# Kernel tuning notes

Measured on AMD Instinct MI355X. Metric: run time of the kernel, lower is better.

Reference implementation:

```python
import jax, jax.numpy as jnp
import numpy as np

B, S, T, D = 16, 512, 16, 128
LN_EPS = 1e-5


def setup_inputs() -> dict:
    key = jax.random.key(0)
    k_x, k_h, k_w = jax.random.split(key, 3)
    x = jax.random.normal(k_x, (B, S, T, D), dtype=jnp.float32)
    # prev_hidden must be strictly positive (code takes its log)
    prev_hidden = jax.random.uniform(k_h, (B, 1, T, D), dtype=jnp.float32) * 0.9 + 0.05
    ln_gamma = jnp.ones((D,), jnp.float32)
    ln_beta = jnp.zeros((D,), jnp.float32)
    # torch Linear(dim, 2*dim): store as (D, 2D) for x @ W
    W = jax.random.normal(k_w, (D, 2 * D), dtype=jnp.float32) * (1.0 / np.sqrt(D))
    b = jnp.zeros((2 * D,), jnp.float32)
    return {"x": x, "prev_hidden": prev_hidden, "ln_gamma": ln_gamma,
            "ln_beta": ln_beta, "W": W, "b": b}


def _g_act_log(h):
    # log of G activation: x>=0 -> log(relu(x)+0.5); x<0 -> -softplus(-x)
    return jnp.where(h >= 0, jnp.log(jax.nn.relu(h) + 0.5), -jax.nn.softplus(-h))


def reference(x, prev_hidden, ln_gamma, ln_beta, W, b):
    seq_len = x.shape[1]
    # LayerNorm over last dim
    mu = jnp.mean(x, axis=-1, keepdims=True)
    var = jnp.var(x, axis=-1, keepdims=True)
    xn = (x - mu) * jax.lax.rsqrt(var + LN_EPS) * ln_gamma + ln_beta
    gh = jnp.einsum('bstd,de->bste', xn, W) + b  # (B,S,T,2D)
    gate, hidden = jnp.split(gh, 2, axis=-1)
    # parallel (seq_len > 1) log-space path
    log_coeffs = -jax.nn.softplus(gate)          # log(1 - z)
    log_z = -jax.nn.softplus(-gate)              # log z
    log_values = log_z + _g_act_log(hidden)      # (B,S,T,D)
    # prepend prev_hidden: values get log(h0), coeffs get zero pad
    log_values = jnp.concatenate([jnp.log(prev_hidden), log_values], axis=1)
    zero_pad = jnp.zeros_like(log_coeffs[:, :1])
    log_coeffs = jnp.concatenate([zero_pad, log_coeffs], axis=1)
    # Heinsen associative scan in log space
    a_star = jnp.cumsum(log_coeffs, axis=1)
    log_h0_plus_b_star = jax.lax.cumlogsumexp(log_values - a_star, axis=1)
    out = jnp.exp(a_star + log_h0_plus_b_star)
    out = out[:, -seq_len:]
    next_prev_hidden = out[:, -1:]
    return out, next_prev_hidden
```

## Files before the change

kernel.cpp:

```cpp
#include <hip/hip_runtime.h>
#include <hip/hip_bf16.h>
#include <stdint.h>

#define BB 16
#define SS 512
#define TT 16
#define DD 128
#define CH 32
#define NCH (SS/CH)
#define LN_EPS 1e-5f

typedef __attribute__((ext_vector_type(8))) short short8;
typedef __attribute__((ext_vector_type(4))) float f32x4;

static __device__ __forceinline__ unsigned short f2bf(float f) {
    unsigned int u = __float_as_uint(f);
    u += 0x7fffu + ((u >> 16) & 1u);
    return (unsigned short)(u >> 16);
}

static __device__ __forceinline__ uint32_t cvt_pk_bf16(float lo, float hi) {
    uint32_t r;
    asm("v_cvt_pk_bf16_f32 %0, %1, %2" : "=v"(r) : "v"(lo), "v"(hi));
    return r;
}

static __device__ __forceinline__ void dma16(const float* g, unsigned char* l) {
    __builtin_amdgcn_global_load_lds(
        (const __attribute__((address_space(1))) unsigned int*)g,
        (__attribute__((address_space(3))) unsigned int*)l, 16, 0, 0);
}

#define BAR() do {                                            \
    asm volatile("s_waitcnt lgkmcnt(0)" ::: "memory");        \
    __builtin_amdgcn_s_barrier();                             \
    asm volatile("" ::: "memory");                            \
} while (0)

__global__ __launch_bounds__(256) void k0_pack(
    const float* __restrict__ W, const float* __restrict__ gamma,
    const float* __restrict__ beta, const float* __restrict__ bias,
    unsigned short* __restrict__ wf, float* __restrict__ bp)
{
    if (blockIdx.x < 128) {
        const int id   = blockIdx.x * 256 + threadIdx.x;
        const int j    = id & 7;
        const int lane = (id >> 3) & 63;
        const int kt   = (id >> 9) & 3;
        const int nt   = (id >> 11) & 15;
        const int col  = nt*16 + (lane & 15);
        const int k    = kt*32 + (lane >> 4)*8 + j;
        wf[id] = f2bf(gamma[k] * W[(size_t)k*256 + col]);
    } else {
        const int col = threadIdx.x;
        float s = bias[col];
        #pragma unroll 8
        for (int k = 0; k < 128; ++k)
            s = fmaf(beta[k], W[(size_t)k*256 + col], s);
        bp[col] = s;
    }
}

__global__ __launch_bounds__(768, 1) void fused_mingru(
    const float* __restrict__ x, const float* __restrict__ prevh,
    const unsigned short* __restrict__ wfrag, const float* __restrict__ bp,
    float* __restrict__ out, float* __restrict__ nexth)
{
    __shared__ __align__(16) unsigned char Xb[3][CH*512];
    __shared__ __align__(16) unsigned char xnb[2][CH*256];
    __shared__ __align__(16) float2 cvb[2][CH][DD];

    const int tid  = threadIdx.x;
    const int w    = tid >> 6;
    const int lane = tid & 63;
    const int l15  = lane & 15;
    const int lhi  = lane >> 4;

    const size_t rowstride = (size_t)TT * DD;
    const size_t base_bt   = ((size_t)(blockIdx.x >> 4) * SS * TT + (blockIdx.x & 15)) * DD;

    const int gw = w - 4;
    short8 wfr[2][4];
    float  bs2[2];
    if (w >= 4) {
        #pragma unroll
        for (int ni = 0; ni < 2; ++ni) {
            const int nt = ni ? (8 + gw) : gw;
            #pragma unroll
            for (int kt = 0; kt < 4; ++kt)
                wfr[ni][kt] = *(const short8*)(wfrag + (size_t)(((nt*4+kt)*64 + lane)*8));
        }
        bs2[0] = bp[gw*16 + l15];
        bs2[1] = bp[128 + gw*16 + l15];
    }

    float h = 0.0f;
    if (tid < 128) h = prevh[(size_t)blockIdx.x * 128 + tid];

    const int tid2 = tid & 127;
    const int r_a  = tid2 >> 2;
    const int q_a  = tid2 & 3;
    const int rx   = r_a & 7;

    auto stageX = [&](int ch) {
        unsigned char* dst = Xb[ch % 3];
        const int j0 = (w == 2) ? 0 : 8;
        #pragma unroll
        for (int jj = 0; jj < 8; ++jj) {
            const int j  = j0 + jj;
            const int r  = 2*j + (lane >> 5);
            const int cc = lane & 31;
            const float* src = x + base_bt + (size_t)(ch*CH + r)*rowstride
                                 + (((cc ^ (r & 7)) << 2));
            dma16(src, dst + j*1024);
        }
    };

    auto phaseLN = [&](int st) {
        const unsigned char* xr = Xb[st % 3] + r_a*512;
        f32x4 vv[8];
        #pragma unroll
        for (int k = 0; k < 8; ++k)
            vv[k] = *(const f32x4*)(xr + (((q_a*8 + k) ^ rx) << 4));
        float s1 = 0.f, s2 = 0.f;
        #pragma unroll
        for (int k = 0; k < 8; ++k) {
            s1 += vv[k].x + vv[k].y + vv[k].z + vv[k].w;
            s2 += vv[k].x*vv[k].x + vv[k].y*vv[k].y + vv[k].z*vv[k].z + vv[k].w*vv[k].w;
        }
        s1 += __shfl_xor(s1, 1); s2 += __shfl_xor(s2, 1);
        s1 += __shfl_xor(s1, 2); s2 += __shfl_xor(s2, 2);
        const float mu = s1 * (1.0f/128.0f);
        const float rs = rsqrtf(s2 * (1.0f/128.0f) - mu*mu + LN_EPS);
        unsigned char* row = xnb[st & 1] + r_a*256;
        #pragma unroll
        for (int m = 0; m < 4; ++m) {
            const f32x4 a = vv[2*m], b = vv[2*m+1];
            union { short8 s8; uint32_t u[4]; } sv;
            sv.u[0] = cvt_pk_bf16((a.x - mu)*rs, (a.y - mu)*rs);
            sv.u[1] = cvt_pk_bf16((a.z - mu)*rs, (a.w - mu)*rs);
            sv.u[2] = cvt_pk_bf16((b.x - mu)*rs, (b.y - mu)*rs);
            sv.u[3] = cvt_pk_bf16((b.z - mu)*rs, (b.w - mu)*rs);
            *(short8*)(row + (((q_a*4 + m) ^ rx) << 4)) = sv.s8;
        }
    };

    auto phaseG = [&](int st) {
        const int bx = st & 1;
        #pragma unroll
        for (int mt = 0; mt < 2; ++mt) {
            const unsigned char* rowp = xnb[bx] + (mt*16 + l15)*256;
            short8 af[4];
            #pragma unroll
            for (int kt = 0; kt < 4; ++kt) {
                const int c = (kt << 2) | lhi;
                af[kt] = *(const short8*)(rowp + ((c ^ (l15 & 7)) << 4));
            }
            f32x4 ag = (f32x4)(0.f), ah = (f32x4)(0.f);
            #pragma unroll
            for (int kt = 0; kt < 4; ++kt) {
                ag = __builtin_amdgcn_mfma_f32_16x16x32_bf16(af[kt], wfr[0][kt], ag, 0, 0, 0);
                ah = __builtin_amdgcn_mfma_f32_16x16x32_bf16(af[kt], wfr[1][kt], ah, 0, 0, 0);
            }
            const int d = gw*16 + l15;
            #pragma unroll
            for (int j = 0; j < 4; ++j) {
                const int ls = mt*16 + lhi*4 + j;
                const float g  = ag[j] + bs2[0];
                const float hh = ah[j] + bs2[1];
                const float c  = 1.0f / (1.0f + __expf(g));
                const float ga = (hh >= 0.0f) ? (hh + 0.5f)
                                              : (1.0f / (1.0f + __expf(-hh)));
                cvb[bx][ls][d] = make_float2(c, (1.0f - c) * ga);
            }
        }
    };

    auto phaseC = [&](int st) {
        const int bc = st & 1;
        float* op = out + base_bt + (size_t)st * CH * rowstride + tid;
        #pragma unroll 8
        for (int ls = 0; ls < CH; ++ls) {
            const float2 cv = cvb[bc][ls][tid];
            h = fmaf(cv.x, h, cv.y);
            op[(size_t)ls * rowstride] = h;
        }
    };

    if (w == 2 || w == 3) { stageX(0); stageX(1); }

    for (int st = 0; st <= NCH + 1; ++st) {
        if (w >= 4) {
            if (st >= 1 && st <= NCH) phaseG(st - 1);
        } else if (w >= 2) {
            if (st < NCH) {
                if (st + 1 < NCH) asm volatile("s_waitcnt vmcnt(8)" ::: "memory");
                else              asm volatile("s_waitcnt vmcnt(0)" ::: "memory");
                phaseLN(st);
                if (st + 2 < NCH) stageX(st + 2);
            }
        } else {
            if (st >= 2) phaseC(st - 2);
        }
        BAR();
    }
    if (tid < 128) nexth[(size_t)blockIdx.x * 128 + tid] = h;
}

extern "C" void kernel_launch(void* const* d_in, const int* in_sizes, int n_in,
                              void* d_out, int out_size, void* d_ws, size_t ws_size,
                              hipStream_t stream) {
    const float* x     = (const float*)d_in[0];
    const float* prevh = (const float*)d_in[1];
    const float* gamma = (const float*)d_in[2];
    const float* beta  = (const float*)d_in[3];
    const float* W     = (const float*)d_in[4];
    const float* bias  = (const float*)d_in[5];

    float* out   = (float*)d_out;
    float* nexth = out + (size_t)BB*SS*TT*DD;

    unsigned short* wf  = (unsigned short*)d_ws;
    float*          bpf = (float*)((char*)d_ws + 65536);

    k0_pack<<<129, 256, 0, stream>>>(W, gamma, beta, bias, wf, bpf);
    fused_mingru<<<BB*TT, 768, 0, stream>>>(x, prevh, wf, bpf, out, nexth);
}
```

Before: 47.59 us.

## Fuse weight packing into main kernel and do scan in registers via MFMA lanes

```diff
diff --git a/kernel.cpp b/kernel.cpp
--- a/kernel.cpp
+++ b/kernel.cpp
@@ -6,29 +6,17 @@
 #define SS 512
 #define TT 16
 #define DD 128
-#define CH 32
+#define CH 64
 #define NCH (SS/CH)
 #define LN_EPS 1e-5f
 
 typedef __attribute__((ext_vector_type(8))) short short8;
 typedef __attribute__((ext_vector_type(4))) float f32x4;
 
-static __device__ __forceinline__ unsigned short f2bf(float f) {
-    unsigned int u = __float_as_uint(f);
-    u += 0x7fffu + ((u >> 16) & 1u);
-    return (unsigned short)(u >> 16);
-}
-
 static __device__ __forceinline__ uint32_t cvt_pk_bf16(float lo, float hi) {
     uint32_t r;
     asm("v_cvt_pk_bf16_f32 %0, %1, %2" : "=v"(r) : "v"(lo), "v"(hi));
     return r;
-}
-
-static __device__ __forceinline__ void dma16(const float* g, unsigned char* l) {
-    __builtin_amdgcn_global_load_lds(
-        (const __attribute__((address_space(1))) unsigned int*)g,
-        (__attribute__((address_space(3))) unsigned int*)l, 16, 0, 0);
 }
 
 #define BAR() do {                                            \
@@ -37,38 +25,13 @@
     asm volatile("" ::: "memory");                            \
 } while (0)
 
-__global__ __launch_bounds__(256) void k0_pack(
-    const float* __restrict__ W, const float* __restrict__ gamma,
-    const float* __restrict__ beta, const float* __restrict__ bias,
-    unsigned short* __restrict__ wf, float* __restrict__ bp)
-{
-    if (blockIdx.x < 128) {
-        const int id   = blockIdx.x * 256 + threadIdx.x;
-        const int j    = id & 7;
-        const int lane = (id >> 3) & 63;
-        const int kt   = (id >> 9) & 3;
-        const int nt   = (id >> 11) & 15;
-        const int col  = nt*16 + (lane & 15);
-        const int k    = kt*32 + (lane >> 4)*8 + j;
-        wf[id] = f2bf(gamma[k] * W[(size_t)k*256 + col]);
-    } else {
-        const int col = threadIdx.x;
-        float s = bias[col];
-        #pragma unroll 8
-        for (int k = 0; k < 128; ++k)
-            s = fmaf(beta[k], W[(size_t)k*256 + col], s);
-        bp[col] = s;
-    }
-}
-
-__global__ __launch_bounds__(768, 1) void fused_mingru(
+__global__ __launch_bounds__(512, 2) void fused_mingru(
     const float* __restrict__ x, const float* __restrict__ prevh,
-    const unsigned short* __restrict__ wfrag, const float* __restrict__ bp,
+    const float* __restrict__ gamma, const float* __restrict__ beta,
+    const float* __restrict__ W, const float* __restrict__ bias,
     float* __restrict__ out, float* __restrict__ nexth)
 {
-    __shared__ __align__(16) unsigned char Xb[3][CH*512];
     __shared__ __align__(16) unsigned char xnb[2][CH*256];
-    __shared__ __align__(16) float2 cvb[2][CH][DD];
 
     const int tid  = threadIdx.x;
     const int w    = tid >> 6;
@@ -76,80 +39,83 @@
     const int l15  = lane & 15;
     const int lhi  = lane >> 4;
 
+    const int bt = blockIdx.x;
     const size_t rowstride = (size_t)TT * DD;
-    const size_t base_bt   = ((size_t)(blockIdx.x >> 4) * SS * TT + (blockIdx.x & 15)) * DD;
+    const size_t base_bt   = ((size_t)(bt >> 4) * SS * TT + (bt & 15)) * DD;
 
-    const int gw = w - 4;
+    const int r_ln  = tid >> 3;
+    const int c8    = tid & 7;
+    const int rx_ln = r_ln & 7;
+    const float* xp0 = x + base_bt + (size_t)r_ln * rowstride + c8*16;
+
+    f32x4 px0, px1, px2, px3;
+    auto issuePx = [&](int st) {
+        const float* xp = xp0 + (size_t)st * CH * rowstride;
+        px0 = *(const f32x4*)(xp + 0);
+        px1 = *(const f32x4*)(xp + 4);
+        px2 = *(const f32x4*)(xp + 8);
+        px3 = *(const f32x4*)(xp + 12);
+    };
+    issuePx(0);
+
     short8 wfr[2][4];
     float  bs2[2];
-    if (w >= 4) {
+    #pragma unroll
+    for (int ni = 0; ni < 2; ++ni) {
+        const int col = (ni ? 128 : 0) + w*16 + l15;
+        float acc = 0.0f;
         #pragma unroll
-        for (int ni = 0; ni < 2; ++ni) {
-            const int nt = ni ? (8 + gw) : gw;
+        for (int kt = 0; kt < 4; ++kt) {
+            union { short8 s8; uint32_t u[4]; } fr;
             #pragma unroll
-            for (int kt = 0; kt < 4; ++kt)
-                wfr[ni][kt] = *(const short8*)(wfrag + (size_t)(((nt*4+kt)*64 + lane)*8));
+            for (int p = 0; p < 4; ++p) {
+                const int k0 = kt*32 + lhi*8 + 2*p;
+                const float w0 = W[(size_t)k0*256 + col];
+                const float w1 = W[(size_t)(k0+1)*256 + col];
+                acc = fmaf(beta[k0],   w0, acc);
+                acc = fmaf(beta[k0+1], w1, acc);
+                fr.u[p] = cvt_pk_bf16(gamma[k0]*w0, gamma[k0+1]*w1);
+            }
+            wfr[ni][kt] = fr.s8;
         }
-        bs2[0] = bp[gw*16 + l15];
-        bs2[1] = bp[128 + gw*16 + l15];
+        acc += __shfl_xor(acc, 16);
+        acc += __shfl_xor(acc, 32);
+        bs2[ni] = bias[col] + acc;
     }
 
-    float h = 0.0f;
-    if (tid < 128) h = prevh[(size_t)blockIdx.x * 128 + tid];
-
-    const int tid2 = tid & 127;
-    const int r_a  = tid2 >> 2;
-    const int q_a  = tid2 & 3;
-    const int rx   = r_a & 7;
-
-    auto stageX = [&](int ch) {
-        unsigned char* dst = Xb[ch % 3];
-        const int j0 = (w == 2) ? 0 : 8;
-        #pragma unroll
-        for (int jj = 0; jj < 8; ++jj) {
-            const int j  = j0 + jj;
-            const int r  = 2*j + (lane >> 5);
-            const int cc = lane & 31;
-            const float* src = x + base_bt + (size_t)(ch*CH + r)*rowstride
-                                 + (((cc ^ (r & 7)) << 2));
-            dma16(src, dst + j*1024);
-        }
-    };
+    float hM = prevh[(size_t)bt*128 + w*16 + l15];
 
     auto phaseLN = [&](int st) {
-        const unsigned char* xr = Xb[st % 3] + r_a*512;
-        f32x4 vv[8];
-        #pragma unroll
-        for (int k = 0; k < 8; ++k)
-            vv[k] = *(const f32x4*)(xr + (((q_a*8 + k) ^ rx) << 4));
-        float s1 = 0.f, s2 = 0.f;
-        #pragma unroll
-        for (int k = 0; k < 8; ++k) {
-            s1 += vv[k].x + vv[k].y + vv[k].z + vv[k].w;
-            s2 += vv[k].x*vv[k].x + vv[k].y*vv[k].y + vv[k].z*vv[k].z + vv[k].w*vv[k].w;
-        }
+        float s1 = px0.x+px0.y+px0.z+px0.w + px1.x+px1.y+px1.z+px1.w
+                 + px2.x+px2.y+px2.z+px2.w + px3.x+px3.y+px3.z+px3.w;
+        float s2 = px0.x*px0.x+px0.y*px0.y+px0.z*px0.z+px0.w*px0.w
+                 + px1.x*px1.x+px1.y*px1.y+px1.z*px1.z+px1.w*px1.w
+                 + px2.x*px2.x+px2.y*px2.y+px2.z*px2.z+px2.w*px2.w
+                 + px3.x*px3.x+px3.y*px3.y+px3.z*px3.z+px3.w*px3.w;
         s1 += __shfl_xor(s1, 1); s2 += __shfl_xor(s2, 1);
         s1 += __shfl_xor(s1, 2); s2 += __shfl_xor(s2, 2);
+        s1 += __shfl_xor(s1, 4); s2 += __shfl_xor(s2, 4);
         const float mu = s1 * (1.0f/128.0f);
         const float rs = rsqrtf(s2 * (1.0f/128.0f) - mu*mu + LN_EPS);
-        unsigned char* row = xnb[st & 1] + r_a*256;
-        #pragma unroll
-        for (int m = 0; m < 4; ++m) {
-            const f32x4 a = vv[2*m], b = vv[2*m+1];
-            union { short8 s8; uint32_t u[4]; } sv;
-            sv.u[0] = cvt_pk_bf16((a.x - mu)*rs, (a.y - mu)*rs);
-            sv.u[1] = cvt_pk_bf16((a.z - mu)*rs, (a.w - mu)*rs);
-            sv.u[2] = cvt_pk_bf16((b.x - mu)*rs, (b.y - mu)*rs);
-            sv.u[3] = cvt_pk_bf16((b.z - mu)*rs, (b.w - mu)*rs);
-            *(short8*)(row + (((q_a*4 + m) ^ rx) << 4)) = sv.s8;
-        }
+        unsigned char* row = xnb[st & 1] + r_ln*256;
+        union { short8 s8; uint32_t u[4]; } a, b2;
+        a.u[0]  = cvt_pk_bf16((px0.x-mu)*rs, (px0.y-mu)*rs);
+        a.u[1]  = cvt_pk_bf16((px0.z-mu)*rs, (px0.w-mu)*rs);
+        a.u[2]  = cvt_pk_bf16((px1.x-mu)*rs, (px1.y-mu)*rs);
+        a.u[3]  = cvt_pk_bf16((px1.z-mu)*rs, (px1.w-mu)*rs);
+        b2.u[0] = cvt_pk_bf16((px2.x-mu)*rs, (px2.y-mu)*rs);
+        b2.u[1] = cvt_pk_bf16((px2.z-mu)*rs, (px2.w-mu)*rs);
+        b2.u[2] = cvt_pk_bf16((px3.x-mu)*rs, (px3.y-mu)*rs);
+        b2.u[3] = cvt_pk_bf16((px3.z-mu)*rs, (px3.w-mu)*rs);
+        *(short8*)(row + (((2*c8)     ^ rx_ln) << 4)) = a.s8;
+        *(short8*)(row + (((2*c8 + 1) ^ rx_ln) << 4)) = b2.s8;
     };
 
     auto phaseG = [&](int st) {
-        const int bx = st & 1;
+        const unsigned char* xb = xnb[st & 1];
         #pragma unroll
-        for (int mt = 0; mt < 2; ++mt) {
-            const unsigned char* rowp = xnb[bx] + (mt*16 + l15)*256;
+        for (int mt = 0; mt < 4; ++mt) {
+            const unsigned char* rowp = xb + (mt*16 + l15)*256;
             short8 af[4];
             #pragma unroll
             for (int kt = 0; kt < 4; ++kt) {
@@ -162,49 +128,52 @@
                 ag = __builtin_amdgcn_mfma_f32_16x16x32_bf16(af[kt], wfr[0][kt], ag, 0, 0, 0);
                 ah = __builtin_amdgcn_mfma_f32_16x16x32_bf16(af[kt], wfr[1][kt], ah, 0, 0, 0);
             }
-            const int d = gw*16 + l15;
+            float Lc[4], Lv[4];
             #pragma unroll
             for (int j = 0; j < 4; ++j) {
-                const int ls = mt*16 + lhi*4 + j;
                 const float g  = ag[j] + bs2[0];
                 const float hh = ah[j] + bs2[1];
-                const float c  = 1.0f / (1.0f + __expf(g));
+                const float cc = 1.0f / (1.0f + __expf(g));
                 const float ga = (hh >= 0.0f) ? (hh + 0.5f)
                                               : (1.0f / (1.0f + __expf(-hh)));
-                cvb[bx][ls][d] = make_float2(c, (1.0f - c) * ga);
+                const float vv = (1.0f - cc) * ga;
+                if (j == 0) { Lc[0] = cc; Lv[0] = vv; }
+                else        { Lc[j] = cc * Lc[j-1]; Lv[j] = fmaf(cc, Lv[j-1], vv); }
             }
+            float Ic = Lc[3], Iv = Lv[3];
+            float pc = __shfl_up(Ic, 16), pv = __shfl_up(Iv, 16);
+            if (lhi >= 1) { Iv = fmaf(Ic, pv, Iv); Ic *= pc; }
+            pc = __shfl_up(Ic, 32); pv = __shfl_up(Iv, 32);
+            if (lhi >= 2) { Iv = fmaf(Ic, pv, Iv); Ic *= pc; }
+            float Ec = __shfl_up(Ic, 16), Ev = __shfl_up(Iv, 16);
+            if (lhi == 0) { Ec = 1.0f; Ev = 0.0f; }
+            const float Mc = __shfl(Ic, 48 + l15);
+            const float Mv = __shfl(Iv, 48 + l15);
+            const float hE = fmaf(Ec, hM, Ev);
+            float* op = out + base_bt
+                      + (size_t)(st*CH + mt*16 + lhi*4) * rowstride + w*16 + l15;
+            #pragma unroll
+            for (int j = 0; j < 4; ++j)
+                op[(size_t)j * rowstride] = fmaf(Lc[j], hE, Lv[j]);
+            hM = fmaf(Mc, hM, Mv);
         }
     };
 
-    auto phaseC = [&](int st) {
-        const int bc = st & 1;
-        float* op = out + base_bt + (size_t)st * CH * rowstride + tid;
-        #pragma unroll 8
-        for (int ls = 0; ls < CH; ++ls) {
-            const float2 cv = cvb[bc][ls][tid];
-            h = fmaf(cv.x, h, cv.y);
-            op[(size_t)ls * rowstride] = h;
-        }
-    };
+    phaseLN(0);
+    issuePx(1);
+    BAR();
 
-    if (w == 2 || w == 3) { stageX(0); stageX(1); }
-
-    for (int st = 0; st <= NCH + 1; ++st) {
-        if (w >= 4) {
-            if (st >= 1 && st <= NCH) phaseG(st - 1);
-        } else if (w >= 2) {
-            if (st < NCH) {
-                if (st + 1 < NCH) asm volatile("s_waitcnt vmcnt(8)" ::: "memory");
-                else              asm volatile("s_waitcnt vmcnt(0)" ::: "memory");
-                phaseLN(st);
-                if (st + 2 < NCH) stageX(st + 2);
-            }
-        } else {
-            if (st >= 2) phaseC(st - 2);
+    for (int st = 0; st < NCH; ++st) {
+        phaseG(st);
+        if (st + 1 < NCH) {
+            phaseLN(st + 1);
+            if (st + 2 < NCH) issuePx(st + 2);
         }
         BAR();
     }
-    if (tid < 128) nexth[(size_t)blockIdx.x * 128 + tid] = h;
+
+    if (lane < 16)
+        nexth[(size_t)bt*128 + w*16 + lane] = hM;
 }
 
 extern "C" void kernel_launch(void* const* d_in, const int* in_sizes, int n_in,
@@ -220,9 +189,6 @@
     float* out   = (float*)d_out;
     float* nexth = out + (size_t)BB*SS*TT*DD;
 
-    unsigned short* wf  = (unsigned short*)d_ws;
-    float*          bpf = (float*)((char*)d_ws + 65536);
-
-    k0_pack<<<129, 256, 0, stream>>>(W, gamma, beta, bias, wf, bpf);
-    fused_mingru<<<BB*TT, 768, 0, stream>>>(x, prevh, wf, bpf, out, nexth);
+    fused_mingru<<<BB*TT, 512, 0, stream>>>(x, prevh, gamma, beta, W, bias,
+                                            out, nexth);
 }
```

Result: faster. 42.91 us (-9.8%).
